# Kernel optimization log

Hardware: AMD Instinct MI355X
Metric: run time of the kernel (lower is better)

The kernel has to match this reference:

```python
import jax, jax.numpy as jnp
import numpy as np
import math

D_MODEL = 1024
N_HEADS = 16
D_K = D_MODEL // N_HEADS


def setup_inputs() -> dict:
    key = jax.random.key(0)
    k1, k2, k3 = jax.random.split(key, 3)
    scale = 1.0 / math.sqrt(D_MODEL)
    return {
        "x": jax.random.normal(k1, (2, 2048, D_MODEL), dtype=jnp.float32),
        "W_qkv": jax.random.normal(k2, (D_MODEL, 3 * D_MODEL), dtype=jnp.float32) * scale,
        "b_qkv": jnp.zeros((3 * D_MODEL,), dtype=jnp.float32),
        "W_out": jax.random.normal(k3, (D_MODEL, D_MODEL), dtype=jnp.float32) * scale,
        "b_out": jnp.zeros((D_MODEL,), dtype=jnp.float32),
    }


def reference(x, W_qkv, b_qkv, W_out, b_out):
    B, S, _ = x.shape
    qkv = x @ W_qkv + b_qkv                      # [B,S,3*D]
    q, k, v = jnp.split(qkv, 3, axis=-1)
    # [B,S,D] -> [B,H,S,d_k]
    def heads(t):
        return t.reshape(B, S, N_HEADS, D_K).transpose(0, 2, 1, 3)
    q, k, v = heads(q), heads(k), heads(v)
    scores = jnp.einsum("bhqd,bhkd->bhqk", q, k) / math.sqrt(D_K)
    attn = jax.nn.softmax(scores, axis=-1)       # [B,H,S,S]
    out = jnp.einsum("bhqk,bhkd->bhqd", attn, v)
    out = out.transpose(0, 2, 1, 3).reshape(B, S, D_MODEL)
    return out @ W_out + b_out
```

## Files before the change

### kernel.cpp

```cpp
#include <hip/hip_runtime.h>
#include <hip/hip_bf16.h>
#include <stdint.h>

#define S_LEN 2048
#define DM    1024
#define NH    16
#define DKH   64
#define BATCH 2
#define M_ROWS (BATCH * S_LEN)
#define NQKV   (3 * DM)

typedef short          bf16x8v __attribute__((ext_vector_type(8)));
typedef float          f32x4   __attribute__((ext_vector_type(4)));
typedef float          f32x16  __attribute__((ext_vector_type(16)));
typedef unsigned short u16x4   __attribute__((ext_vector_type(4)));
typedef unsigned short u16x8   __attribute__((ext_vector_type(8)));
typedef unsigned int   u32x2   __attribute__((ext_vector_type(2)));
typedef unsigned int   u32x4   __attribute__((ext_vector_type(4)));

typedef const void __attribute__((address_space(1))) gas_void;
typedef void       __attribute__((address_space(3))) las_void;

static __device__ __forceinline__ unsigned short f2bf(float f) {
    union { float f; uint32_t u; } v; v.f = f;
    uint32_t u = v.u;
    uint32_t r = (u + 0x7fffu + ((u >> 16) & 1u)) >> 16;
    return (unsigned short)r;
}

static __device__ __forceinline__ float exp2_hw(float x) {
    float r;
    asm("v_exp_f32 %0, %1" : "=v"(r) : "v"(x));
    return r;
}

static __device__ __forceinline__ uint32_t cvtpk_bf16(float lo, float hi) {
    uint32_t r;
    asm("v_cvt_pk_bf16_f32 %0, %1, %2" : "=v"(r) : "v"(lo), "v"(hi));
    return r;
}
static __device__ __forceinline__ u32x2 pl32swap(uint32_t a, uint32_t b) {
    return __builtin_amdgcn_permlane32_swap(a, b, false, false);
}
static __device__ __forceinline__ float    fbits(uint32_t u) { return __builtin_bit_cast(float, u); }
static __device__ __forceinline__ uint32_t ubits(float f)    { return __builtin_bit_cast(uint32_t, f); }

__global__ __launch_bounds__(256) void cvt_bf16_kernel(
    const float* __restrict__ in, unsigned short* __restrict__ out, int n8)
{
    const int i = blockIdx.x * 256 + threadIdx.x;
    if (i >= n8) return;
    f32x4 a = *(const f32x4*)(in + (size_t)i * 8);
    f32x4 b = *(const f32x4*)(in + (size_t)i * 8 + 4);
    u16x8 o;
    #pragma unroll
    for (int j = 0; j < 4; ++j) { o[j] = f2bf(a[j]); o[4 + j] = f2bf(b[j]); }
    *(u16x8*)(out + (size_t)i * 8) = o;
}

__global__ __launch_bounds__(256) void transpose_w_kernel(
    const float* __restrict__ W, unsigned short* __restrict__ Wt, int K, int N)
{
    __shared__ float t[32][33];
    const int tx = threadIdx.x, ty = threadIdx.y;
    const int n0 = blockIdx.x * 32, k0 = blockIdx.y * 32;
    #pragma unroll
    for (int i = 0; i < 4; ++i)
        t[ty * 4 + i][tx] = W[(size_t)(k0 + ty * 4 + i) * N + n0 + tx];
    __syncthreads();
    #pragma unroll
    for (int i = 0; i < 4; ++i)
        Wt[(size_t)(n0 + ty * 4 + i) * K + k0 + tx] = f2bf(t[tx][ty * 4 + i]);
}

template <int EPI>
__global__ __launch_bounds__(256) void gemm_bt_kernel(
    const unsigned short* __restrict__ A, const unsigned short* __restrict__ Bt,
    const float* __restrict__ bias, void* __restrict__ Cout,
    int M, int N, int K)
{
    __shared__ __attribute__((aligned(16))) unsigned short As[128 * 32];
    __shared__ __attribute__((aligned(16))) unsigned short Bs[128 * 32];

    const int tid  = threadIdx.x;
    const int lane = tid & 63;
    const int w    = tid >> 6;
    const int wr   = w >> 1, wc = w & 1;
    const int lr   = lane & 15, lg = lane >> 4;
    const int m0   = blockIdx.y * 128, n0 = blockIdx.x * 128;

    f32x4 acc[4][4];
    #pragma unroll
    for (int i = 0; i < 4; ++i)
        #pragma unroll
        for (int j = 0; j < 4; ++j) acc[i][j] = (f32x4){0.f, 0.f, 0.f, 0.f};

    for (int kt = 0; kt < K; kt += 32) {
        if (kt) __syncthreads();
        #pragma unroll
        for (int j = 0; j < 2; ++j) {
            const int c  = j * 256 + tid;
            const int r  = c >> 2;
            const int kc = (c & 3) * 8;
            const int cb = j * 256 + (tid & ~63);
            __builtin_amdgcn_global_load_lds(
                (gas_void*)(A + (size_t)(m0 + r) * K + kt + kc),
                (las_void*)((char*)As + (size_t)cb * 16), 16, 0, 0);
            __builtin_amdgcn_global_load_lds(
                (gas_void*)(Bt + (size_t)(n0 + r) * K + kt + kc),
                (las_void*)((char*)Bs + (size_t)cb * 16), 16, 0, 0);
        }
        __syncthreads();

        bf16x8v af[4], bfv[4];
        #pragma unroll
        for (int mi = 0; mi < 4; ++mi)
            af[mi] = *(const bf16x8v*)(&As[(wr * 64 + mi * 16 + lr) * 32 + lg * 8]);
        #pragma unroll
        for (int ni = 0; ni < 4; ++ni)
            bfv[ni] = *(const bf16x8v*)(&Bs[(wc * 64 + ni * 16 + lr) * 32 + lg * 8]);
        #pragma unroll
        for (int mi = 0; mi < 4; ++mi)
            #pragma unroll
            for (int ni = 0; ni < 4; ++ni)
                acc[mi][ni] = __builtin_amdgcn_mfma_f32_16x16x32_bf16(
                    af[mi], bfv[ni], acc[mi][ni], 0, 0, 0);
    }

    const int grow0 = m0 + wr * 64 + lg * 4;
    const int gcol0 = n0 + wc * 64 + lr;
    #pragma unroll
    for (int mi = 0; mi < 4; ++mi)
        #pragma unroll
        for (int ni = 0; ni < 4; ++ni) {
            const int gcol = gcol0 + ni * 16;
            const float bv = bias[gcol];
            #pragma unroll
            for (int r = 0; r < 4; ++r) {
                const size_t idx = (size_t)(grow0 + mi * 16 + r) * N + gcol;
                const float v = acc[mi][ni][r] + bv;
                if (EPI == 0) ((unsigned short*)Cout)[idx] = f2bf(v);
                else          ((float*)Cout)[idx] = v;
            }
        }
}

__global__ __launch_bounds__(256) void split_v_kernel(
    const unsigned short* __restrict__ qkv, unsigned short* __restrict__ vt)
{
    const int tid = threadIdx.x;
    const int bh  = blockIdx.y;
    const int h   = bh & 15;
    const int b   = bh >> 4;
    const int s0  = blockIdx.x * 64;
    __shared__ __attribute__((aligned(16))) unsigned short tile[64][68];

    #pragma unroll
    for (int j = 0; j < 4; ++j) {
        const int c  = tid + j * 256;
        const int r  = c >> 4;
        const int c4 = (c & 15) * 4;
        const size_t srow = ((size_t)b * S_LEN + s0 + r) * NQKV + 2 * DM + h * 64 + c4;
        *(u16x4*)&tile[r][c4] = *(const u16x4*)(qkv + srow);
    }
    __syncthreads();
    #pragma unroll
    for (int j = 0; j < 4; ++j) {
        const int c   = tid + j * 256;
        const int dkr = c >> 4;
        const int s4  = (c & 15) * 4;
        u16x4 o;
        #pragma unroll
        for (int i = 0; i < 4; ++i) o[i] = tile[s4 + i][dkr];
        *(u16x4*)(vt + ((size_t)bh * DKH + dkr) * S_LEN + s0 + s4) = o;
    }
}

#define EXP_C1 0.18033688f
#define KVB 64

static __device__ __forceinline__ int swzkey(int r) { return (r ^ (r >> 3)) & 7; }

#define LDS_SUB_STEP(KsB, VsB, ks)                                                   \
do {                                                                                 \
                         \
    bf16x8v kc_[4], vc_[4];                                                          \
    _Pragma("unroll")                                                                \
    for (int s_ = 0; s_ < 4; ++s_) {                                                 \
        const int r_ = (ks) + lo;                                                    \
        kc_[s_] = *(const bf16x8v*)((KsB) + r_ * 128 +                               \
                                    (((s_ * 2 + hi) ^ swzkey(r_)) << 4));            \
    }                                                                                \
    _Pragma("unroll")                                                                \
    for (int j_ = 0; j_ < 4; ++j_) {                                                 \
        const int r_ = (j_ >> 1) * 32 + lo;                                          \
        const int cc_ = ((ks) >> 3) + (j_ & 1) * 2 + hi;                             \
        vc_[j_] = *(const bf16x8v*)((VsB) + r_ * 128 +                               \
                                    ((cc_ ^ swzkey(r_)) << 4));                      \
    }                                                                                \
    f32x16 scA = {}, scB = {};                                                       \
    __builtin_amdgcn_s_setprio(1);                                                   \
    scA = __builtin_amdgcn_mfma_f32_32x32x16_bf16(kc_[0], qf[0], scA, 0, 0, 0);      \
    scB = __builtin_amdgcn_mfma_f32_32x32x16_bf16(kc_[1], qf[1], scB, 0, 0, 0);      \
    scA = __builtin_amdgcn_mfma_f32_32x32x16_bf16(kc_[2], qf[2], scA, 0, 0, 0);      \
    scB = __builtin_amdgcn_mfma_f32_32x32x16_bf16(kc_[3], qf[3], scB, 0, 0, 0);      \
    __builtin_amdgcn_s_setprio(0);                                                   \
    f32x16 sc = scA + scB;                                                           \
                                \
    float pe_[16];                                                                   \
    _Pragma("unroll")                                                                \
    for (int r_ = 0; r_ < 16; ++r_)                                                  \
        pe_[r_] = exp2_hw(sc[r_] * EXP_C1);                                          \
    float u0_ = (pe_[0] + pe_[1]) + (pe_[2] + pe_[3]);                               \
    float u1_ = (pe_[4] + pe_[5]) + (pe_[6] + pe_[7]);                               \
    float u2_ = (pe_[8] + pe_[9]) + (pe_[10] + pe_[11]);                             \
    float u3_ = (pe_[12] + pe_[13]) + (pe_[14] + pe_[15]);                           \
    float ss_ = (u0_ + u1_) + (u2_ + u3_);                                           \
    { u32x2 sw_ = pl32swap(ubits(ss_), ubits(ss_));                                  \
      ss_ = fbits(sw_[0]) + fbits(sw_[1]); }                                         \
    lsum += ss_;                                                                     \
             \
    uint32_t a01_ = cvtpk_bf16(pe_[0],  pe_[1]),  a23_ = cvtpk_bf16(pe_[2],  pe_[3]);  \
    uint32_t a45_ = cvtpk_bf16(pe_[4],  pe_[5]),  a67_ = cvtpk_bf16(pe_[6],  pe_[7]);  \
    uint32_t b01_ = cvtpk_bf16(pe_[8],  pe_[9]),  b23_ = cvtpk_bf16(pe_[10], pe_[11]); \
    uint32_t b45_ = cvtpk_bf16(pe_[12], pe_[13]), b67_ = cvtpk_bf16(pe_[14], pe_[15]); \
    u32x2 s0_ = pl32swap(a01_, a45_);                                                \
    u32x2 s1_ = pl32swap(a23_, a67_);                                                \
    u32x2 s2_ = pl32swap(b01_, b45_);                                                \
    u32x2 s3_ = pl32swap(b23_, b67_);                                                \
    u32x4 w0_ = { s0_[0], s1_[0], s0_[1], s1_[1] };                                  \
    u32x4 w1_ = { s2_[0], s3_[0], s2_[1], s3_[1] };                                  \
    bf16x8v pa0_ = __builtin_bit_cast(bf16x8v, w0_);                                 \
    bf16x8v pa1_ = __builtin_bit_cast(bf16x8v, w1_);                                 \
    __builtin_amdgcn_s_setprio(1);                                                   \
    acc0 = __builtin_amdgcn_mfma_f32_32x32x16_bf16(vc_[0], pa0_, acc0, 0, 0, 0);     \
    acc0 = __builtin_amdgcn_mfma_f32_32x32x16_bf16(vc_[1], pa1_, acc0, 0, 0, 0);     \
    acc1 = __builtin_amdgcn_mfma_f32_32x32x16_bf16(vc_[2], pa0_, acc1, 0, 0, 0);     \
    acc1 = __builtin_amdgcn_mfma_f32_32x32x16_bf16(vc_[3], pa1_, acc1, 0, 0, 0);     \
    __builtin_amdgcn_s_setprio(0);                                                   \
} while (0)

__global__ __launch_bounds__(256, 2) void attn_kernel(
    const unsigned short* __restrict__ QKV, const unsigned short* __restrict__ Vt,
    unsigned short* __restrict__ O)
{
    const int tid  = threadIdx.x;
    const int w    = tid >> 6;
    const int lane = tid & 63;
    const int lo = lane & 31;
    const int hi = lane >> 5;

    const int flat = blockIdx.x;
    const int virt = (flat & 7) * 64 + (flat >> 3);
    const int bh = virt >> 4;
    const int qb = virt & 15;
    const int b = bh >> 4, h = bh & 15;
    const int q0 = qb * 128 + w * 32;

    __shared__ __attribute__((aligned(16))) unsigned short Ks[2][KVB * 64];
    __shared__ __attribute__((aligned(16))) unsigned short Vs[2][KVB * 64];

    const unsigned short* Kq  = QKV + (size_t)b * S_LEN * NQKV + DM + h * 64;
    const unsigned short* Vtb = Vt + (size_t)bh * DKH * S_LEN;

    const int sr  = tid >> 3, scn = tid & 7;
    const size_t kSrc0 = (size_t)sr * NQKV + ((scn ^ swzkey(sr)) * 8);
    const size_t kSrc1 = (size_t)(sr + 32) * NQKV + ((scn ^ swzkey(sr + 32)) * 8);
    const size_t vSrc0 = (size_t)sr * S_LEN + ((scn ^ swzkey(sr)) * 8);
    const size_t vSrc1 = (size_t)(sr + 32) * S_LEN + ((scn ^ swzkey(sr + 32)) * 8);
    const int dstOff0 = (tid & ~63) * 16;
    const int dstOff1 = dstOff0 + 4096;

#define STAGE_TILE(buf, kvOff)                                                        \
    do {                                                                              \
        __builtin_amdgcn_global_load_lds((gas_void*)(Kq + (kvOff) * NQKV + kSrc0),    \
            (las_void*)((char*)&Ks[buf][0] + dstOff0), 16, 0, 0);                     \
        __builtin_amdgcn_global_load_lds((gas_void*)(Kq + (kvOff) * NQKV + kSrc1),    \
            (las_void*)((char*)&Ks[buf][0] + dstOff1), 16, 0, 0);                     \
        __builtin_amdgcn_global_load_lds((gas_void*)(Vtb + (kvOff) + vSrc0),          \
            (las_void*)((char*)&Vs[buf][0] + dstOff0), 16, 0, 0);                     \
        __builtin_amdgcn_global_load_lds((gas_void*)(Vtb + (kvOff) + vSrc1),          \
            (las_void*)((char*)&Vs[buf][0] + dstOff1), 16, 0, 0);                     \
    } while (0)

    const unsigned short* Qp =
        QKV + ((size_t)b * S_LEN + q0 + lo) * NQKV + h * 64 + hi * 8;
    bf16x8v qf[4];
    #pragma unroll
    for (int s = 0; s < 4; ++s) qf[s] = *(const bf16x8v*)(Qp + s * 16);

    f32x16 acc0 = {}, acc1 = {};
    float lsum = 0.f;

    STAGE_TILE(0, (size_t)0);
    __syncthreads();

    int cur = 0;
    for (int t = 0; t < S_LEN / KVB; ++t) {
        const int nxt = cur ^ 1;
        if (t + 1 < S_LEN / KVB) STAGE_TILE(nxt, (size_t)(t + 1) * KVB);
        const char* KsB = (const char*)&Ks[cur][0];
        const char* VsB = (const char*)&Vs[cur][0];
        LDS_SUB_STEP(KsB, VsB, 0);
        LDS_SUB_STEP(KsB, VsB, 32);
        __syncthreads();
        cur = nxt;
    }
#undef STAGE_TILE

    const float linv = 1.f / lsum;
    unsigned short* Orow = O + ((size_t)b * S_LEN + q0 + lo) * DM + h * 64 + hi * 4;
    #pragma unroll
    for (int g = 0; g < 4; ++g) {
        u16x4 st0, st1;
        #pragma unroll
        for (int k2 = 0; k2 < 4; ++k2) {
            st0[k2] = f2bf(acc0[g * 4 + k2] * linv);
            st1[k2] = f2bf(acc1[g * 4 + k2] * linv);
        }
        *(u16x4*)(Orow + g * 8)      = st0;
        *(u16x4*)(Orow + 32 + g * 8) = st1;
    }
}

extern "C" void kernel_launch(void* const* d_in, const int* in_sizes, int n_in,
                              void* d_out, int out_size, void* d_ws, size_t ws_size,
                              hipStream_t stream)
{
    const float* x    = (const float*)d_in[0];
    const float* Wqkv = (const float*)d_in[1];
    const float* bqkv = (const float*)d_in[2];
    const float* Wout = (const float*)d_in[3];
    const float* bout = (const float*)d_in[4];
    float* out = (float*)d_out;

    char* ws = (char*)d_ws;
    unsigned short* xb     = (unsigned short*)(ws);
    unsigned short* wqkv_t = (unsigned short*)(ws + 8388608);
    unsigned short* wout_t = (unsigned short*)(ws + 14680064);
    unsigned short* qkvb   = (unsigned short*)(ws + 16777216);
    unsigned short* attn_o = (unsigned short*)(ws + 41943040);
    unsigned short* vtb    = (unsigned short*)(ws + 50331648);

    cvt_bf16_kernel<<<2048, 256, 0, stream>>>(x, xb, (M_ROWS * DM) / 8);
    transpose_w_kernel<<<dim3(NQKV / 32, DM / 32), dim3(32, 8), 0, stream>>>(Wqkv, wqkv_t, DM, NQKV);
    transpose_w_kernel<<<dim3(DM / 32, DM / 32), dim3(32, 8), 0, stream>>>(Wout, wout_t, DM, DM);
    gemm_bt_kernel<0><<<dim3(NQKV / 128, M_ROWS / 128), 256, 0, stream>>>(
        xb, wqkv_t, bqkv, (void*)qkvb, M_ROWS, NQKV, DM);
    split_v_kernel<<<dim3(S_LEN / 64, BATCH * NH), 256, 0, stream>>>(qkvb, vtb);
    attn_kernel<<<512, 256, 0, stream>>>(qkvb, vtb, attn_o);
    gemm_bt_kernel<1><<<dim3(DM / 128, M_ROWS / 128), 256, 0, stream>>>(
        attn_o, wout_t, bout, (void*)out, M_ROWS, DM, DM);
}
```

Baseline: 129.4 us.

## Split attention KV range across two wave groups per query tile

```diff
diff --git a/kernel.cpp b/kernel.cpp
--- a/kernel.cpp
+++ b/kernel.cpp
@@ -240,12 +240,14 @@
     __builtin_amdgcn_s_setprio(0);                                                   \
 } while (0)
 
-__global__ __launch_bounds__(256, 2) void attn_kernel(
+__global__ __launch_bounds__(512, 2) void attn_kernel(
     const unsigned short* __restrict__ QKV, const unsigned short* __restrict__ Vt,
     unsigned short* __restrict__ O)
 {
     const int tid  = threadIdx.x;
     const int w    = tid >> 6;
+    const int qt   = w >> 1;
+    const int kh   = w & 1;
     const int lane = tid & 63;
     const int lo = lane & 31;
     const int hi = lane >> 5;
@@ -255,32 +257,30 @@
     const int bh = virt >> 4;
     const int qb = virt & 15;
     const int b = bh >> 4, h = bh & 15;
-    const int q0 = qb * 128 + w * 32;
-
-    __shared__ __attribute__((aligned(16))) unsigned short Ks[2][KVB * 64];
-    __shared__ __attribute__((aligned(16))) unsigned short Vs[2][KVB * 64];
+    const int q0 = qb * 128 + qt * 32;
+
+    __shared__ __attribute__((aligned(16))) unsigned short Ks[2][2][KVB * 64];
+    __shared__ __attribute__((aligned(16))) unsigned short Vs[2][2][KVB * 64];
 
     const unsigned short* Kq  = QKV + (size_t)b * S_LEN * NQKV + DM + h * 64;
     const unsigned short* Vtb = Vt + (size_t)bh * DKH * S_LEN;
 
     const int sr  = tid >> 3, scn = tid & 7;
-    const size_t kSrc0 = (size_t)sr * NQKV + ((scn ^ swzkey(sr)) * 8);
-    const size_t kSrc1 = (size_t)(sr + 32) * NQKV + ((scn ^ swzkey(sr + 32)) * 8);
-    const size_t vSrc0 = (size_t)sr * S_LEN + ((scn ^ swzkey(sr)) * 8);
-    const size_t vSrc1 = (size_t)(sr + 32) * S_LEN + ((scn ^ swzkey(sr + 32)) * 8);
-    const int dstOff0 = (tid & ~63) * 16;
-    const int dstOff1 = dstOff0 + 4096;
-
-#define STAGE_TILE(buf, kvOff)                                                        \
+    const size_t kSrc = (size_t)sr * NQKV  + ((scn ^ swzkey(sr)) * 8);
+    const size_t vSrc = (size_t)sr * S_LEN + ((scn ^ swzkey(sr)) * 8);
+    const int dstOff = (tid & ~63) * 16;
+
+#define STAGE_TILE(buf, t)                                                            \
     do {                                                                              \
-        __builtin_amdgcn_global_load_lds((gas_void*)(Kq + (kvOff) * NQKV + kSrc0),    \
-            (las_void*)((char*)&Ks[buf][0] + dstOff0), 16, 0, 0);                     \
-        __builtin_amdgcn_global_load_lds((gas_void*)(Kq + (kvOff) * NQKV + kSrc1),    \
-            (las_void*)((char*)&Ks[buf][0] + dstOff1), 16, 0, 0);                     \
-        __builtin_amdgcn_global_load_lds((gas_void*)(Vtb + (kvOff) + vSrc0),          \
-            (las_void*)((char*)&Vs[buf][0] + dstOff0), 16, 0, 0);                     \
-        __builtin_amdgcn_global_load_lds((gas_void*)(Vtb + (kvOff) + vSrc1),          \
-            (las_void*)((char*)&Vs[buf][0] + dstOff1), 16, 0, 0);                     \
+        const size_t kv0_ = (size_t)(t) * KVB;                                        \
+        __builtin_amdgcn_global_load_lds((gas_void*)(Kq + kv0_ * NQKV + kSrc),        \
+            (las_void*)((char*)&Ks[buf][0][0] + dstOff), 16, 0, 0);                   \
+        __builtin_amdgcn_global_load_lds((gas_void*)(Kq + (kv0_ + 1024) * NQKV + kSrc),\
+            (las_void*)((char*)&Ks[buf][1][0] + dstOff), 16, 0, 0);                   \
+        __builtin_amdgcn_global_load_lds((gas_void*)(Vtb + kv0_ + vSrc),              \
+            (las_void*)((char*)&Vs[buf][0][0] + dstOff), 16, 0, 0);                   \
+        __builtin_amdgcn_global_load_lds((gas_void*)(Vtb + kv0_ + 1024 + vSrc),       \
+            (las_void*)((char*)&Vs[buf][1][0] + dstOff), 16, 0, 0);                   \
     } while (0)
 
     const unsigned short* Qp =
@@ -292,15 +292,15 @@
     f32x16 acc0 = {}, acc1 = {};
     float lsum = 0.f;
 
-    STAGE_TILE(0, (size_t)0);
+    STAGE_TILE(0, 0);
     __syncthreads();
 
     int cur = 0;
-    for (int t = 0; t < S_LEN / KVB; ++t) {
+    for (int t = 0; t < S_LEN / (2 * KVB); ++t) {
         const int nxt = cur ^ 1;
-        if (t + 1 < S_LEN / KVB) STAGE_TILE(nxt, (size_t)(t + 1) * KVB);
-        const char* KsB = (const char*)&Ks[cur][0];
-        const char* VsB = (const char*)&Vs[cur][0];
+        if (t + 1 < S_LEN / (2 * KVB)) STAGE_TILE(nxt, t + 1);
+        const char* KsB = (const char*)&Ks[cur][kh][0];
+        const char* VsB = (const char*)&Vs[cur][kh][0];
         LDS_SUB_STEP(KsB, VsB, 0);
         LDS_SUB_STEP(KsB, VsB, 32);
         __syncthreads();
@@ -308,18 +308,38 @@
     }
 #undef STAGE_TILE
 
-    const float linv = 1.f / lsum;
-    unsigned short* Orow = O + ((size_t)b * S_LEN + q0 + lo) * DM + h * 64 + hi * 4;
-    #pragma unroll
-    for (int g = 0; g < 4; ++g) {
-        u16x4 st0, st1;
-        #pragma unroll
-        for (int k2 = 0; k2 < 4; ++k2) {
-            st0[k2] = f2bf(acc0[g * 4 + k2] * linv);
-            st1[k2] = f2bf(acc1[g * 4 + k2] * linv);
-        }
-        *(u16x4*)(Orow + g * 8)      = st0;
-        *(u16x4*)(Orow + 32 + g * 8) = st1;
+    float* accbuf = (float*)&Ks[0][0][0] + qt * 2048;
+    float* lsbuf  = (float*)&Vs[0][0][0] + qt * 64;
+    if (kh == 1) {
+        #pragma unroll
+        for (int i = 0; i < 16; ++i) {
+            accbuf[i * 64 + lane]        = acc0[i];
+            accbuf[(16 + i) * 64 + lane] = acc1[i];
+        }
+        lsbuf[lane & 63] = lsum;
+    }
+    __syncthreads();
+    if (kh == 0) {
+        #pragma unroll
+        for (int i = 0; i < 16; ++i) {
+            acc0[i] += accbuf[i * 64 + lane];
+            acc1[i] += accbuf[(16 + i) * 64 + lane];
+        }
+        lsum += lsbuf[lane];
+
+        const float linv = 1.f / lsum;
+        unsigned short* Orow = O + ((size_t)b * S_LEN + q0 + lo) * DM + h * 64 + hi * 4;
+        #pragma unroll
+        for (int g = 0; g < 4; ++g) {
+            u16x4 st0, st1;
+            #pragma unroll
+            for (int k2 = 0; k2 < 4; ++k2) {
+                st0[k2] = f2bf(acc0[g * 4 + k2] * linv);
+                st1[k2] = f2bf(acc1[g * 4 + k2] * linv);
+            }
+            *(u16x4*)(Orow + g * 8)      = st0;
+            *(u16x4*)(Orow + 32 + g * 8) = st1;
+        }
     }
 }
 
@@ -348,7 +368,7 @@
     gemm_bt_kernel<0><<<dim3(NQKV / 128, M_ROWS / 128), 256, 0, stream>>>(
         xb, wqkv_t, bqkv, (void*)qkvb, M_ROWS, NQKV, DM);
     split_v_kernel<<<dim3(S_LEN / 64, BATCH * NH), 256, 0, stream>>>(qkvb, vtb);
-    attn_kernel<<<512, 256, 0, stream>>>(qkvb, vtb, attn_o);
+    attn_kernel<<<512, 512, 0, stream>>>(qkvb, vtb, attn_o);
     gemm_bt_kernel<1><<<dim3(DM / 128, M_ROWS / 128), 256, 0, stream>>>(
         attn_o, wout_t, bout, (void*)out, M_ROWS, DM, DM);
 }
```

After: 140.3 us. +8.4%, slower.

## Merge prep kernels and write transposed V directly from QKV GEMM epilogue

Applied to the files above, without the earlier changes.

```diff
diff --git a/kernel.cpp b/kernel.cpp
--- a/kernel.cpp
+++ b/kernel.cpp
@@ -45,25 +45,32 @@
 static __device__ __forceinline__ float    fbits(uint32_t u) { return __builtin_bit_cast(float, u); }
 static __device__ __forceinline__ uint32_t ubits(float f)    { return __builtin_bit_cast(uint32_t, f); }
 
-__global__ __launch_bounds__(256) void cvt_bf16_kernel(
-    const float* __restrict__ in, unsigned short* __restrict__ out, int n8)
+__global__ __launch_bounds__(256) void prep_kernel(
+    const float* __restrict__ x, unsigned short* __restrict__ xb,
+    const float* __restrict__ Wqkv, unsigned short* __restrict__ wqkv_t,
+    const float* __restrict__ Wout, unsigned short* __restrict__ wout_t)
 {
-    const int i = blockIdx.x * 256 + threadIdx.x;
-    if (i >= n8) return;
-    f32x4 a = *(const f32x4*)(in + (size_t)i * 8);
-    f32x4 b = *(const f32x4*)(in + (size_t)i * 8 + 4);
-    u16x8 o;
-    #pragma unroll
-    for (int j = 0; j < 4; ++j) { o[j] = f2bf(a[j]); o[4 + j] = f2bf(b[j]); }
-    *(u16x8*)(out + (size_t)i * 8) = o;
-}
-
-__global__ __launch_bounds__(256) void transpose_w_kernel(
-    const float* __restrict__ W, unsigned short* __restrict__ Wt, int K, int N)
-{
+    const int bid = blockIdx.x;
+    const int tid = threadIdx.x;
     __shared__ float t[32][33];
-    const int tx = threadIdx.x, ty = threadIdx.y;
-    const int n0 = blockIdx.x * 32, k0 = blockIdx.y * 32;
+
+    if (bid < 2048) {
+        const int i = bid * 256 + tid;
+        f32x4 a = *(const f32x4*)(x + (size_t)i * 8);
+        f32x4 b = *(const f32x4*)(x + (size_t)i * 8 + 4);
+        u16x8 o;
+        #pragma unroll
+        for (int j = 0; j < 4; ++j) { o[j] = f2bf(a[j]); o[4 + j] = f2bf(b[j]); }
+        *(u16x8*)(xb + (size_t)i * 8) = o;
+        return;
+    }
+    const float* W; unsigned short* Wt; int N, tb;
+    if (bid < 2048 + 3072) { W = Wqkv; Wt = wqkv_t; N = NQKV; tb = bid - 2048; }
+    else                   { W = Wout; Wt = wout_t; N = DM;   tb = bid - 5120; }
+    const int K  = DM;
+    const int nb = N / 32;
+    const int n0 = (tb % nb) * 32, k0 = (tb / nb) * 32;
+    const int tx = tid & 31, ty = tid >> 5;
     #pragma unroll
     for (int i = 0; i < 4; ++i)
         t[ty * 4 + i][tx] = W[(size_t)(k0 + ty * 4 + i) * N + n0 + tx];
@@ -77,6 +84,7 @@
 __global__ __launch_bounds__(256) void gemm_bt_kernel(
     const unsigned short* __restrict__ A, const unsigned short* __restrict__ Bt,
     const float* __restrict__ bias, void* __restrict__ Cout,
+    unsigned short* __restrict__ vt,
     int M, int N, int K)
 {
     __shared__ __attribute__((aligned(16))) unsigned short As[128 * 32];
@@ -129,6 +137,25 @@
 
     const int grow0 = m0 + wr * 64 + lg * 4;
     const int gcol0 = n0 + wc * 64 + lr;
+    if (EPI == 0 && n0 >= 2 * DM) {
+        #pragma unroll
+        for (int mi = 0; mi < 4; ++mi) {
+            const int grow = grow0 + mi * 16;
+            const int b    = grow >> 11;
+            const int sl   = grow & (S_LEN - 1);
+            #pragma unroll
+            for (int ni = 0; ni < 4; ++ni) {
+                const int gcol = gcol0 + ni * 16;
+                const float bv = bias[gcol];
+                const int dc = gcol - 2 * DM;
+                u16x4 st;
+                #pragma unroll
+                for (int r = 0; r < 4; ++r) st[r] = f2bf(acc[mi][ni][r] + bv);
+                *(u16x4*)(vt + ((size_t)b * NH * DKH + dc) * S_LEN + sl) = st;
+            }
+        }
+        return;
+    }
     #pragma unroll
     for (int mi = 0; mi < 4; ++mi)
         #pragma unroll
@@ -145,37 +172,6 @@
         }
 }
 
-__global__ __launch_bounds__(256) void split_v_kernel(
-    const unsigned short* __restrict__ qkv, unsigned short* __restrict__ vt)
-{
-    const int tid = threadIdx.x;
-    const int bh  = blockIdx.y;
-    const int h   = bh & 15;
-    const int b   = bh >> 4;
-    const int s0  = blockIdx.x * 64;
-    __shared__ __attribute__((aligned(16))) unsigned short tile[64][68];
-
-    #pragma unroll
-    for (int j = 0; j < 4; ++j) {
-        const int c  = tid + j * 256;
-        const int r  = c >> 4;
-        const int c4 = (c & 15) * 4;
-        const size_t srow = ((size_t)b * S_LEN + s0 + r) * NQKV + 2 * DM + h * 64 + c4;
-        *(u16x4*)&tile[r][c4] = *(const u16x4*)(qkv + srow);
-    }
-    __syncthreads();
-    #pragma unroll
-    for (int j = 0; j < 4; ++j) {
-        const int c   = tid + j * 256;
-        const int dkr = c >> 4;
-        const int s4  = (c & 15) * 4;
-        u16x4 o;
-        #pragma unroll
-        for (int i = 0; i < 4; ++i) o[i] = tile[s4 + i][dkr];
-        *(u16x4*)(vt + ((size_t)bh * DKH + dkr) * S_LEN + s0 + s4) = o;
-    }
-}
-
 #define EXP_C1 0.18033688f
 #define KVB 64
 
@@ -183,7 +179,6 @@
 
 #define LDS_SUB_STEP(KsB, VsB, ks)                                                   \
 do {                                                                                 \
-                         \
     bf16x8v kc_[4], vc_[4];                                                          \
     _Pragma("unroll")                                                                \
     for (int s_ = 0; s_ < 4; ++s_) {                                                 \
@@ -206,7 +201,6 @@
     scB = __builtin_amdgcn_mfma_f32_32x32x16_bf16(kc_[3], qf[3], scB, 0, 0, 0);      \
     __builtin_amdgcn_s_setprio(0);                                                   \
     f32x16 sc = scA + scB;                                                           \
-                                \
     float pe_[16];                                                                   \
     _Pragma("unroll")                                                                \
     for (int r_ = 0; r_ < 16; ++r_)                                                  \
@@ -219,7 +213,6 @@
     { u32x2 sw_ = pl32swap(ubits(ss_), ubits(ss_));                                  \
       ss_ = fbits(sw_[0]) + fbits(sw_[1]); }                                         \
     lsum += ss_;                                                                     \
-             \
     uint32_t a01_ = cvtpk_bf16(pe_[0],  pe_[1]),  a23_ = cvtpk_bf16(pe_[2],  pe_[3]);  \
     uint32_t a45_ = cvtpk_bf16(pe_[4],  pe_[5]),  a67_ = cvtpk_bf16(pe_[6],  pe_[7]);  \
     uint32_t b01_ = cvtpk_bf16(pe_[8],  pe_[9]),  b23_ = cvtpk_bf16(pe_[10], pe_[11]); \
@@ -342,13 +335,10 @@
     unsigned short* attn_o = (unsigned short*)(ws + 41943040);
     unsigned short* vtb    = (unsigned short*)(ws + 50331648);
 
-    cvt_bf16_kernel<<<2048, 256, 0, stream>>>(x, xb, (M_ROWS * DM) / 8);
-    transpose_w_kernel<<<dim3(NQKV / 32, DM / 32), dim3(32, 8), 0, stream>>>(Wqkv, wqkv_t, DM, NQKV);
-    transpose_w_kernel<<<dim3(DM / 32, DM / 32), dim3(32, 8), 0, stream>>>(Wout, wout_t, DM, DM);
+    prep_kernel<<<6144, 256, 0, stream>>>(x, xb, Wqkv, wqkv_t, Wout, wout_t);
     gemm_bt_kernel<0><<<dim3(NQKV / 128, M_ROWS / 128), 256, 0, stream>>>(
-        xb, wqkv_t, bqkv, (void*)qkvb, M_ROWS, NQKV, DM);
-    split_v_kernel<<<dim3(S_LEN / 64, BATCH * NH), 256, 0, stream>>>(qkvb, vtb);
+        xb, wqkv_t, bqkv, (void*)qkvb, vtb, M_ROWS, NQKV, DM);
     attn_kernel<<<512, 256, 0, stream>>>(qkvb, vtb, attn_o);
     gemm_bt_kernel<1><<<dim3(DM / 128, M_ROWS / 128), 256, 0, stream>>>(
-        attn_o, wout_t, bout, (void*)out, M_ROWS, DM, DM);
-}
+        attn_o, wout_t, bout, (void*)out, nullptr, M_ROWS, DM, DM);
+}
```

New measurement: 135.4 us. +4.6%, slower.
